# Performance work log

Measured on AMD Instinct MI355X. Metric: run time of the kernel, lower is better.

Reference implementation:

```python
import jax, jax.numpy as jnp
import numpy as np

N_NODES = 50000
N_EDGES = 800000
N_GRAPHS = 512
F_IN = 64
HID = 64
OUT = 1
NUM_LAYERS = 3


def setup_inputs() -> dict:
    key = jax.random.key(0)
    ks = jax.random.split(key, 10)
    x = jax.random.normal(ks[0], (N_NODES, F_IN), dtype=jnp.float32)
    edge_index = jax.random.randint(ks[1], (2, N_EDGES), 0, N_NODES, dtype=jnp.int64)
    batch = jnp.sort(jax.random.randint(ks[2], (N_NODES,), 0, N_GRAPHS, dtype=jnp.int64))
    def glorot(k, shape):
        lim = np.sqrt(6.0 / (shape[0] + shape[1]))
        return jax.random.uniform(k, shape, jnp.float32, -lim, lim)
    W1 = glorot(ks[3], (F_IN, HID))
    b1 = jnp.zeros((HID,), jnp.float32)
    W2 = glorot(ks[4], (HID, HID))
    b2 = jnp.zeros((HID,), jnp.float32)
    Wmem = glorot(ks[5], (HID, OUT))
    bmem = jnp.zeros((OUT,), jnp.float32)
    Wtime = glorot(ks[6], (HID, OUT))
    btime = jnp.zeros((OUT,), jnp.float32)
    return {"x": x, "edge_index": edge_index, "batch": batch,
            "W1": W1, "b1": b1, "W2": W2, "b2": b2,
            "Wmem": Wmem, "bmem": bmem, "Wtime": Wtime, "btime": btime}


def _gcn_forward(x, edge_index, batch, W1, b1, W2, b2, Wmem, bmem, Wtime, btime):
    N = x.shape[0]
    # add self-loops (PyG GCNConv default)
    loop = jnp.arange(N, dtype=edge_index.dtype)
    src = jnp.concatenate([edge_index[0], loop])  # [E+N]
    dst = jnp.concatenate([edge_index[1], loop])
    # symmetric normalization: deg over destination nodes (incl. self-loops)
    deg = jax.ops.segment_sum(jnp.ones_like(dst, dtype=x.dtype), dst, num_segments=N)
    dinv = jnp.where(deg > 0, jax.lax.rsqrt(deg), 0.0)
    norm = (dinv[src] * dinv[dst])[:, None]  # [E+N, 1]

    def conv(h, W, b):
        h = h @ W                                   # transform first (PyG order)
        msg = h[src] * norm                         # gather + normalize
        agg = jax.ops.segment_sum(msg, dst, num_segments=N)  # scatter-add
        return agg + b

    h = jax.nn.relu(conv(x, W1, b1))
    for _ in range(NUM_LAYERS - 1):
        h = jax.nn.relu(conv(h, W2, b2))

    # global_mean_pool over batch index
    sums = jax.ops.segment_sum(h, batch, num_segments=N_GRAPHS)
    cnts = jax.ops.segment_sum(jnp.ones((N,), h.dtype), batch, num_segments=N_GRAPHS)
    pooled = sums / jnp.maximum(cnts, 1.0)[:, None]  # [G, HID]

    mem_pred = (pooled @ Wmem + bmem).squeeze()
    time_pred = (pooled @ Wtime + btime).squeeze()
    return mem_pred, time_pred


def reference(x, edge_index, batch, W1, b1, W2, b2, Wmem, bmem, Wtime, btime):
    return _gcn_forward(x, edge_index, batch, W1, b1, W2, b2, Wmem, bmem, Wtime, btime)
```

## Files before the change

kernel.cpp:

```cpp
#include <hip/hip_runtime.h>
#include <hip/hip_bf16.h>
#include <hip/hip_fp16.h>

#define F 64
#define BSH 7
#define MAXB 512
#define CAPB 4096

typedef short short8 __attribute__((ext_vector_type(8)));
typedef float f32x4  __attribute__((ext_vector_type(4)));

__device__ __forceinline__ unsigned short f2bf(float x) {
    unsigned u = __float_as_uint(x);
    unsigned r = (u + 0x7fff + ((u >> 16) & 1)) >> 16;
    return (unsigned short)r;
}
__device__ __forceinline__ float bf2f(unsigned short h) {
    return __uint_as_float(((unsigned)h) << 16);
}

__global__ void k_prep(const float* __restrict__ W1, const float* __restrict__ W2,
                       short* __restrict__ Wh1, short* __restrict__ Wl1,
                       short* __restrict__ Wh2, short* __restrict__ Wl2,
                       int* __restrict__ bfill,
                       __half* __restrict__ xn, __half* __restrict__ hA,
                       __half* __restrict__ hB, int n,
                       float* __restrict__ pooled, int* __restrict__ cnt, int ng) {
    int b = blockIdx.x, t = threadIdx.x;
    if (b < 4) {
        const float* W = (b < 2) ? W1 : W2;
        short* WhF = (b < 2) ? Wh1 : Wh2;
        short* WlF = (b < 2) ? Wl1 : Wl2;
        int i = (b & 1) * 256 + t;
        int lane = i & 63;
        int ct = i >> 6;
        int tt = ct & 1, c = ct >> 1;
        int j  = c * 16 + (lane & 15);
        int k0 = tt * 32 + (lane >> 4) * 8;
        #pragma unroll
        for (int e = 0; e < 8; ++e) {
            float xv = W[(k0 + e) * F + j];
            unsigned short hi = f2bf(xv);
            WhF[i * 8 + e] = (short)hi;
            WlF[i * 8 + e] = (short)f2bf(xv - bf2f(hi));
        }
    } else if (b == 4) {
        bfill[t]       = t * CAPB;
        bfill[t + 256] = (t + 256) * CAPB;
    } else if (b == 5) {
        if (t < 32)      ((unsigned*)(xn + (size_t)n * F))[t]      = 0u;
        else if (t < 64) ((unsigned*)(hA + (size_t)n * F))[t - 32] = 0u;
        else if (t < 96) ((unsigned*)(hB + (size_t)n * F))[t - 64] = 0u;
    } else {
        int idx = (b - 6) * 256 + t;
        if (idx < ng * F) pooled[idx] = 0.f;
        else if (idx < ng * F + ng) cnt[idx - ng * F] = 0;
    }
}

__global__ void k_binscatter(const int* __restrict__ src, const int* __restrict__ dst,
                             int e, int nbkt, int* __restrict__ bucket_fill,
                             int* __restrict__ binned) {
    __shared__ int h[MAXB], base[MAXB];
    int t = threadIdx.x;
    int perblk = (e + gridDim.x - 1) / gridDim.x;
    int e0 = blockIdx.x * perblk;
    int e1 = min(e0 + perblk, e);
    for (int i = t; i < nbkt; i += 256) h[i] = 0;
    __syncthreads();
    for (int i = e0 + t; i < e1; i += 256) atomicAdd(&h[dst[i] >> BSH], 1);
    __syncthreads();
    for (int i = t; i < nbkt; i += 256) {
        int c = h[i];
        base[i] = c ? atomicAdd(&bucket_fill[i], c) : 0;
        h[i] = 0;
    }
    __syncthreads();
    for (int i = e0 + t; i < e1; i += 256) {
        int d = dst[i];
        int b = d >> BSH;
        int r = atomicAdd(&h[b], 1);
        binned[base[b] + r] = (src[i] << BSH) | (d & ((1 << BSH) - 1));
    }
}

__global__ void k_bincsr(const int* __restrict__ binned, const int* __restrict__ bfill,
                         const float* __restrict__ x, int n,
                         int* __restrict__ csr, int2* __restrict__ rowse,
                         float* __restrict__ dinv, __half* __restrict__ xn) {
    __shared__ int deg[1 << BSH], dp[1 << BSH], rp[1 << BSH], fill[1 << BSH];
    __shared__ int csr_l[CAPB];
    __shared__ int ovf;
    int b = blockIdx.x;
    int t = threadIdx.x;
    int n0 = b << BSH;
    int nn = min(n - n0, 1 << BSH);
    if (nn <= 0) return;
    int base = b * CAPB;
    int cnt = bfill[b] - base;
    if (t < (1 << BSH)) { deg[t] = 0; fill[t] = 0; }
    for (int i = t; i < CAPB; i += 256) csr_l[i] = n;
    __syncthreads();
    for (int i = t; i < cnt; i += 256) atomicAdd(&deg[binned[base + i] & ((1 << BSH) - 1)], 1);
    __syncthreads();
    if (t < 128) { dp[t] = (deg[t] + 15) & ~15; rp[t] = dp[t]; }
    __syncthreads();
    for (int off = 1; off < 128; off <<= 1) {
        int u = 0;
        if (t < 128 && t >= off) u = rp[t - off];
        __syncthreads();
        if (t < 128) rp[t] += u;
        __syncthreads();
    }
    if (t == 0) ovf = (rp[127] > CAPB);
    __syncthreads();
    if (ovf) {
        if (t < 128) { dp[t] = deg[t]; rp[t] = deg[t]; }
        __syncthreads();
        for (int off = 1; off < 128; off <<= 1) {
            int u = 0;
            if (t < 128 && t >= off) u = rp[t - off];
            __syncthreads();
            if (t < 128) rp[t] += u;
            __syncthreads();
        }
    }
    int total = rp[127];
    for (int i = t; i < cnt; i += 256) {
        int pr = binned[base + i];
        int d = pr & ((1 << BSH) - 1);
        int pos = rp[d] - dp[d] + atomicAdd(&fill[d], 1);
        csr_l[pos] = pr >> BSH;
    }
    __syncthreads();
    for (int i = t; i < total; i += 256) csr[base + i] = csr_l[i];
    if (t < nn) {
        int start = base + rp[t] - dp[t];
        rowse[n0 + t] = make_int2(start, start + dp[t]);
        dinv[n0 + t]  = rsqrtf((float)(deg[t] + 1));
    }
    for (int i = t; i < nn * 32; i += 256) {
        int r = i >> 5, l = i & 31;
        float dv = rsqrtf((float)(deg[r] + 1));
        float2 v = ((const float2*)(x + (size_t)(n0 + r) * F))[l];
        ((__half2*)(xn + (size_t)(n0 + r) * F))[l] = __floats2half2_rn(v.x * dv, v.y * dv);
    }
}

template<int SCALE_OUT>
__global__ __launch_bounds__(256, 8)
void k_layer(const __half* __restrict__ Hn, const int2* __restrict__ rowse,
             const int* __restrict__ csr, const float* __restrict__ dinv,
             const short* __restrict__ WhF, const short* __restrict__ WlF,
             const float* __restrict__ bias, __half* __restrict__ out, int n) {
    __shared__ short Ah[16][72];
    __shared__ short Al[16][72];
    __shared__ float sdinv[16];
    int t  = threadIdx.x;
    int w  = t >> 6, t6 = t & 63;
    int g  = t6 >> 5, l = t6 & 31;
    int nb0 = blockIdx.x * 16;
    const __half2* rows = (const __half2*)Hn;

    for (int q = 0; q < 4; ++q) {
        int ndl = w * 4 + q;
        int nd  = nb0 + ndl;
        float ax[8], ay[8];
        #pragma unroll
        for (int i = 0; i < 8; ++i) { ax[i] = 0.f; ay[i] = 0.f; }
        float dn = 0.f;
        if (nd < n) {
            dn = dinv[nd];
            if (g == 0) {
                float2 f = __half22float2(rows[((size_t)nd << 5) + l]);
                ax[0] = f.x; ay[0] = f.y;
            }
            int2 se = rowse[nd];
            int e = se.x, e1 = se.y;
            if ((e & 15) == 0) {
                for (; e + 16 <= e1; e += 16) {
                    const int4* cp = (const int4*)(csr + e + 8 * g);
                    int4 c0 = cp[0], c1 = cp[1];
                    int s[8] = {c0.x, c0.y, c0.z, c0.w, c1.x, c1.y, c1.z, c1.w};
                    #pragma unroll
                    for (int i = 0; i < 8; ++i) {
                        float2 f = __half22float2(rows[((size_t)s[i] << 5) + l]);
                        ax[i] += f.x; ay[i] += f.y;
                    }
                }
            }
            if (g == 0) {
                for (; e < e1; ++e) {
                    int s = csr[e];
                    float2 f = __half22float2(rows[((size_t)s << 5) + l]);
                    ax[7] += f.x; ay[7] += f.y;
                }
            }
        }
        float sx = ((ax[0] + ax[1]) + (ax[2] + ax[3])) + ((ax[4] + ax[5]) + (ax[6] + ax[7]));
        float sy = ((ay[0] + ay[1]) + (ay[2] + ay[3])) + ((ay[4] + ay[5]) + (ay[6] + ay[7]));
        sx += __shfl_xor(sx, 32);
        sy += __shfl_xor(sy, 32);
        sx *= dn; sy *= dn;
        if (g == 0) {
            unsigned short hx = f2bf(sx), hy = f2bf(sy);
            *(unsigned*)&Ah[ndl][2 * l] = (unsigned)hx | ((unsigned)hy << 16);
            unsigned short lx = f2bf(sx - bf2f(hx)), ly = f2bf(sy - bf2f(hy));
            *(unsigned*)&Al[ndl][2 * l] = (unsigned)lx | ((unsigned)ly << 16);
            if (l == 0) sdinv[ndl] = dn;
        }
    }
    __syncthreads();

    int c  = w;
    int jj = t6 & 15;
    int kg = t6 >> 4;
    const short8* WhP = (const short8*)WhF;
    const short8* WlP = (const short8*)WlF;
    short8 bh0 = WhP[(c * 2 + 0) * 64 + t6];
    short8 bh1 = WhP[(c * 2 + 1) * 64 + t6];
    short8 bl0 = WlP[(c * 2 + 0) * 64 + t6];
    short8 bl1 = WlP[(c * 2 + 1) * 64 + t6];
    short8 ah0 = *(const short8*)&Ah[jj][kg * 8];
    short8 ah1 = *(const short8*)&Ah[jj][32 + kg * 8];
    short8 al0 = *(const short8*)&Al[jj][kg * 8];
    short8 al1 = *(const short8*)&Al[jj][32 + kg * 8];

    float bv = bias[c * 16 + jj];
    f32x4 acc = {bv, bv, bv, bv};
    acc = __builtin_amdgcn_mfma_f32_16x16x32_bf16(ah0, bh0, acc, 0, 0, 0);
    acc = __builtin_amdgcn_mfma_f32_16x16x32_bf16(ah1, bh1, acc, 0, 0, 0);
    acc = __builtin_amdgcn_mfma_f32_16x16x32_bf16(al0, bh0, acc, 0, 0, 0);
    acc = __builtin_amdgcn_mfma_f32_16x16x32_bf16(al1, bh1, acc, 0, 0, 0);
    acc = __builtin_amdgcn_mfma_f32_16x16x32_bf16(ah0, bl0, acc, 0, 0, 0);
    acc = __builtin_amdgcn_mfma_f32_16x16x32_bf16(ah1, bl1, acc, 0, 0, 0);

    #pragma unroll
    for (int v = 0; v < 4; ++v) {
        int rr = kg * 4 + v;
        int nd = nb0 + rr;
        if (nd < n) {
            float val = fmaxf(acc[v], 0.f);
            if (SCALE_OUT) val *= sdinv[rr];
            out[(size_t)nd * F + c * 16 + jj] = __float2half(val);
        }
    }
}


#define POOL_C 32
__global__ void k_pool(const __half* __restrict__ h, const int* __restrict__ batch,
                       float* __restrict__ pooled, int* __restrict__ cnt, int n) {
    int wave = (blockIdx.x * blockDim.x + threadIdx.x) >> 6;
    int j = threadIdx.x & 63;
    int n0 = wave * POOL_C;
    if (n0 >= n) return;
    int n1 = min(n0 + POOL_C, n);
    int curg = batch[n0];
    float acc = 0.f; int c = 0;
    for (int i = n0; i < n1; ++i) {
        int g = batch[i];
        if (g != curg) {
            atomicAdd(&pooled[curg * F + j], acc);
            if (j == 0) atomicAdd(&cnt[curg], c);
            curg = g; acc = 0.f; c = 0;
        }
        acc += __half2float(h[(size_t)i * F + j]);
        ++c;
    }
    atomicAdd(&pooled[curg * F + j], acc);
    if (j == 0) atomicAdd(&cnt[curg], c);
}

__global__ void k_head(const float* __restrict__ pooled, const int* __restrict__ cnt,
                       const float* __restrict__ Wm, const float* __restrict__ bm,
                       const float* __restrict__ Wt, const float* __restrict__ bt,
                       float* __restrict__ out, int g) {
    int gid = (blockIdx.x * blockDim.x + threadIdx.x) >> 6;
    int j = threadIdx.x & 63;
    if (gid >= g) return;
    float c = fmaxf((float)cnt[gid], 1.f);
    float p = pooled[gid * F + j] / c;
    float m = p * Wm[j];
    float t = p * Wt[j];
    #pragma unroll
    for (int off = 32; off > 0; off >>= 1) {
        m += __shfl_down(m, off);
        t += __shfl_down(t, off);
    }
    if (j == 0) {
        out[gid]     = m + bm[0];
        out[g + gid] = t + bt[0];
    }
}


static inline size_t alignup(size_t x) { return (x + 255) & ~(size_t)255; }

extern "C" void kernel_launch(void* const* d_in, const int* in_sizes, int n_in,
                              void* d_out, int out_size, void* d_ws, size_t ws_size,
                              hipStream_t stream) {
    const float* x     = (const float*)d_in[0];
    const int*   eidx  = (const int*)d_in[1];
    const int*   batch = (const int*)d_in[2];
    const float* W1    = (const float*)d_in[3];
    const float* b1    = (const float*)d_in[4];
    const float* W2    = (const float*)d_in[5];
    const float* b2    = (const float*)d_in[6];
    const float* Wm    = (const float*)d_in[7];
    const float* bm    = (const float*)d_in[8];
    const float* Wt    = (const float*)d_in[9];
    const float* bt    = (const float*)d_in[10];
    float* out = (float*)d_out;

    const int N = in_sizes[0] / F;
    const int E = in_sizes[1] / 2;
    const int G = out_size / 2;
    const int* src = eidx;
    const int* dst = eidx + E;
    const int nbkt = (N + (1 << BSH) - 1) >> BSH;

    char* p = (char*)d_ws;
    float*  dinv   = (float*)p;  p += alignup(sizeof(float) * N);
    int2*   rowse  = (int2*)p;   p += alignup(sizeof(int2) * N);
    int*    bfill  = (int*)p;    p += alignup(sizeof(int) * MAXB);
    short*  Wh1    = (short*)p;  p += alignup(sizeof(short) * 4096);
    short*  Wl1    = (short*)p;  p += alignup(sizeof(short) * 4096);
    short*  Wh2    = (short*)p;  p += alignup(sizeof(short) * 4096);
    short*  Wl2    = (short*)p;  p += alignup(sizeof(short) * 4096);
    int*    csr    = (int*)p;    p += alignup(sizeof(int) * (size_t)nbkt * CAPB);
    int*    binned = (int*)p;    p += alignup(sizeof(int) * (size_t)nbkt * CAPB);
    __half* xn     = (__half*)p; p += alignup(sizeof(__half) * (size_t)(N + 1) * F);
    __half* hA     = (__half*)p; p += alignup(sizeof(__half) * (size_t)(N + 1) * F);
    __half* hB     = (__half*)p; p += alignup(sizeof(__half) * (size_t)(N + 1) * F);
    float*  pooled = (float*)p;  p += alignup(sizeof(float) * G * F);
    int*    cnt    = (int*)p;    p += alignup(sizeof(int) * G);

    const int TB = 256;

    int gPrep = 6 + (G * F + G + TB - 1) / TB;
    k_prep<<<gPrep, TB, 0, stream>>>(W1, W2, Wh1, Wl1, Wh2, Wl2, bfill,
                                     xn, hA, hB, N, pooled, cnt, G);

    k_binscatter<<<128, TB, 0, stream>>>(src, dst, E, nbkt, bfill, binned);
    k_bincsr    <<<nbkt, TB, 0, stream>>>(binned, bfill, x, N, csr, rowse, dinv, xn);

    int gT = (N + 15) / 16;
    k_layer<1><<<gT, TB, 0, stream>>>(xn, rowse, csr, dinv, Wh1, Wl1, b1, hA, N);
    k_layer<1><<<gT, TB, 0, stream>>>(hA, rowse, csr, dinv, Wh2, Wl2, b2, hB, N);
    k_layer<0><<<gT, TB, 0, stream>>>(hB, rowse, csr, dinv, Wh2, Wl2, b2, hA, N);

    int pw = (N + POOL_C - 1) / POOL_C;
    k_pool<<<(pw * 64 + TB - 1) / TB, TB, 0, stream>>>(hA, batch, pooled, cnt, N);
    int gH = (G * F + TB - 1) / TB;
    k_head<<<gH, TB, 0, stream>>>(pooled, cnt, Wm, bm, Wt, bt, out, G);
}
```

Baseline: 136.7 us.

## Fuse mean pooling into last GCN layer and store CSR indices as uint16

The final layer kernel now applies ReLU, stages its 16 output rows in shared memory and atomically adds per-graph sums and counts. This removes the separate pooling kernel and the write and re-read of the last hidden state. The CSR neighbor indices are also narrowed from 32-bit to 16-bit, halving index traffic in the gather loops. The narrowing only holds while the node count stays below 65536, and the fused pooling issues more atomics per graph than the old pooling kernel did.

```diff
diff --git a/kernel.cpp b/kernel.cpp
--- a/kernel.cpp
+++ b/kernel.cpp
@@ -9,6 +9,7 @@
 
 typedef short short8 __attribute__((ext_vector_type(8)));
 typedef float f32x4  __attribute__((ext_vector_type(4)));
+typedef unsigned short ushort_t;
 
 __device__ __forceinline__ unsigned short f2bf(float x) {
     unsigned u = __float_as_uint(x);
@@ -86,7 +87,7 @@
 
 __global__ void k_bincsr(const int* __restrict__ binned, const int* __restrict__ bfill,
                          const float* __restrict__ x, int n,
-                         int* __restrict__ csr, int2* __restrict__ rowse,
+                         ushort_t* __restrict__ csr, int2* __restrict__ rowse,
                          float* __restrict__ dinv, __half* __restrict__ xn) {
     __shared__ int deg[1 << BSH], dp[1 << BSH], rp[1 << BSH], fill[1 << BSH];
     __shared__ int csr_l[CAPB];
@@ -133,7 +134,7 @@
         csr_l[pos] = pr >> BSH;
     }
     __syncthreads();
-    for (int i = t; i < total; i += 256) csr[base + i] = csr_l[i];
+    for (int i = t; i < total; i += 256) csr[base + i] = (ushort_t)csr_l[i];
     if (t < nn) {
         int start = base + rp[t] - dp[t];
         rowse[n0 + t] = make_int2(start, start + dp[t]);
@@ -147,14 +148,20 @@
     }
 }
 
-template<int SCALE_OUT>
+union SMem {
+    struct { short Ah[16][72]; short Al[16][72]; };
+    struct { float vals[16][68]; int bids[16]; };
+};
+
+template<int MODE>
 __global__ __launch_bounds__(256, 8)
 void k_layer(const __half* __restrict__ Hn, const int2* __restrict__ rowse,
-             const int* __restrict__ csr, const float* __restrict__ dinv,
+             const ushort_t* __restrict__ csr, const float* __restrict__ dinv,
              const short* __restrict__ WhF, const short* __restrict__ WlF,
-             const float* __restrict__ bias, __half* __restrict__ out, int n) {
-    __shared__ short Ah[16][72];
-    __shared__ short Al[16][72];
+             const float* __restrict__ bias, __half* __restrict__ out,
+             const int* __restrict__ batch, float* __restrict__ pooled,
+             int* __restrict__ cnt, int n) {
+    __shared__ SMem sm;
     __shared__ float sdinv[16];
     int t  = threadIdx.x;
     int w  = t >> 6, t6 = t & 63;
@@ -179,9 +186,11 @@
             int e = se.x, e1 = se.y;
             if ((e & 15) == 0) {
                 for (; e + 16 <= e1; e += 16) {
-                    const int4* cp = (const int4*)(csr + e + 8 * g);
-                    int4 c0 = cp[0], c1 = cp[1];
-                    int s[8] = {c0.x, c0.y, c0.z, c0.w, c1.x, c1.y, c1.z, c1.w};
+                    int4 cw = *(const int4*)(csr + e + 8 * g);
+                    int s[8] = { cw.x & 0xffff, (int)((unsigned)cw.x >> 16),
+                                 cw.y & 0xffff, (int)((unsigned)cw.y >> 16),
+                                 cw.z & 0xffff, (int)((unsigned)cw.z >> 16),
+                                 cw.w & 0xffff, (int)((unsigned)cw.w >> 16) };
                     #pragma unroll
                     for (int i = 0; i < 8; ++i) {
                         float2 f = __half22float2(rows[((size_t)s[i] << 5) + l]);
@@ -204,9 +213,9 @@
         sx *= dn; sy *= dn;
         if (g == 0) {
             unsigned short hx = f2bf(sx), hy = f2bf(sy);
-            *(unsigned*)&Ah[ndl][2 * l] = (unsigned)hx | ((unsigned)hy << 16);
+            *(unsigned*)&sm.Ah[ndl][2 * l] = (unsigned)hx | ((unsigned)hy << 16);
             unsigned short lx = f2bf(sx - bf2f(hx)), ly = f2bf(sy - bf2f(hy));
-            *(unsigned*)&Al[ndl][2 * l] = (unsigned)lx | ((unsigned)ly << 16);
+            *(unsigned*)&sm.Al[ndl][2 * l] = (unsigned)lx | ((unsigned)ly << 16);
             if (l == 0) sdinv[ndl] = dn;
         }
     }
@@ -221,10 +230,10 @@
     short8 bh1 = WhP[(c * 2 + 1) * 64 + t6];
     short8 bl0 = WlP[(c * 2 + 0) * 64 + t6];
     short8 bl1 = WlP[(c * 2 + 1) * 64 + t6];
-    short8 ah0 = *(const short8*)&Ah[jj][kg * 8];
-    short8 ah1 = *(const short8*)&Ah[jj][32 + kg * 8];
-    short8 al0 = *(const short8*)&Al[jj][kg * 8];
-    short8 al1 = *(const short8*)&Al[jj][32 + kg * 8];
+    short8 ah0 = *(const short8*)&sm.Ah[jj][kg * 8];
+    short8 ah1 = *(const short8*)&sm.Ah[jj][32 + kg * 8];
+    short8 al0 = *(const short8*)&sm.Al[jj][kg * 8];
+    short8 al1 = *(const short8*)&sm.Al[jj][32 + kg * 8];
 
     float bv = bias[c * 16 + jj];
     f32x4 acc = {bv, bv, bv, bv};
@@ -235,42 +244,51 @@
     acc = __builtin_amdgcn_mfma_f32_16x16x32_bf16(ah0, bl0, acc, 0, 0, 0);
     acc = __builtin_amdgcn_mfma_f32_16x16x32_bf16(ah1, bl1, acc, 0, 0, 0);
 
-    #pragma unroll
-    for (int v = 0; v < 4; ++v) {
-        int rr = kg * 4 + v;
-        int nd = nb0 + rr;
-        if (nd < n) {
-            float val = fmaxf(acc[v], 0.f);
-            if (SCALE_OUT) val *= sdinv[rr];
-            out[(size_t)nd * F + c * 16 + jj] = __float2half(val);
-        }
-    }
-}
-
-
-#define POOL_C 32
-__global__ void k_pool(const __half* __restrict__ h, const int* __restrict__ batch,
-                       float* __restrict__ pooled, int* __restrict__ cnt, int n) {
-    int wave = (blockIdx.x * blockDim.x + threadIdx.x) >> 6;
-    int j = threadIdx.x & 63;
-    int n0 = wave * POOL_C;
-    if (n0 >= n) return;
-    int n1 = min(n0 + POOL_C, n);
-    int curg = batch[n0];
-    float acc = 0.f; int c = 0;
-    for (int i = n0; i < n1; ++i) {
-        int g = batch[i];
-        if (g != curg) {
-            atomicAdd(&pooled[curg * F + j], acc);
-            if (j == 0) atomicAdd(&cnt[curg], c);
-            curg = g; acc = 0.f; c = 0;
-        }
-        acc += __half2float(h[(size_t)i * F + j]);
-        ++c;
-    }
-    atomicAdd(&pooled[curg * F + j], acc);
-    if (j == 0) atomicAdd(&cnt[curg], c);
-}
+    if (MODE == 1) {
+        #pragma unroll
+        for (int v = 0; v < 4; ++v) {
+            int rr = kg * 4 + v;
+            int nd = nb0 + rr;
+            if (nd < n) {
+                float val = fmaxf(acc[v], 0.f) * sdinv[rr];
+                out[(size_t)nd * F + c * 16 + jj] = __float2half(val);
+            }
+        }
+    } else {
+        __syncthreads();
+        #pragma unroll
+        for (int v = 0; v < 4; ++v) {
+            int rr = kg * 4 + v;
+            sm.vals[rr][c * 16 + jj] = fmaxf(acc[v], 0.f);
+        }
+        if (t < 16) sm.bids[t] = (nb0 + t < n) ? batch[nb0 + t] : -1;
+        __syncthreads();
+        if (t < 64) {
+            float accp = 0.f;
+            int curg = sm.bids[0];
+            for (int r = 0; r < 16; ++r) {
+                int g2 = sm.bids[r];
+                if (g2 < 0) break;
+                if (g2 != curg) {
+                    atomicAdd(&pooled[curg * F + t], accp);
+                    curg = g2; accp = 0.f;
+                }
+                accp += sm.vals[r][t];
+            }
+            if (curg >= 0) atomicAdd(&pooled[curg * F + t], accp);
+        } else if (t == 64) {
+            int curg = sm.bids[0], cl = 0;
+            for (int r = 0; r < 16; ++r) {
+                int g2 = sm.bids[r];
+                if (g2 < 0) break;
+                if (g2 != curg) { atomicAdd(&cnt[curg], cl); curg = g2; cl = 0; }
+                ++cl;
+            }
+            if (curg >= 0 && cl) atomicAdd(&cnt[curg], cl);
+        }
+    }
+}
+
 
 __global__ void k_head(const float* __restrict__ pooled, const int* __restrict__ cnt,
                        const float* __restrict__ Wm, const float* __restrict__ bm,
@@ -321,20 +339,20 @@
     const int nbkt = (N + (1 << BSH) - 1) >> BSH;
 
     char* p = (char*)d_ws;
-    float*  dinv   = (float*)p;  p += alignup(sizeof(float) * N);
-    int2*   rowse  = (int2*)p;   p += alignup(sizeof(int2) * N);
-    int*    bfill  = (int*)p;    p += alignup(sizeof(int) * MAXB);
-    short*  Wh1    = (short*)p;  p += alignup(sizeof(short) * 4096);
-    short*  Wl1    = (short*)p;  p += alignup(sizeof(short) * 4096);
-    short*  Wh2    = (short*)p;  p += alignup(sizeof(short) * 4096);
-    short*  Wl2    = (short*)p;  p += alignup(sizeof(short) * 4096);
-    int*    csr    = (int*)p;    p += alignup(sizeof(int) * (size_t)nbkt * CAPB);
-    int*    binned = (int*)p;    p += alignup(sizeof(int) * (size_t)nbkt * CAPB);
-    __half* xn     = (__half*)p; p += alignup(sizeof(__half) * (size_t)(N + 1) * F);
-    __half* hA     = (__half*)p; p += alignup(sizeof(__half) * (size_t)(N + 1) * F);
-    __half* hB     = (__half*)p; p += alignup(sizeof(__half) * (size_t)(N + 1) * F);
-    float*  pooled = (float*)p;  p += alignup(sizeof(float) * G * F);
-    int*    cnt    = (int*)p;    p += alignup(sizeof(int) * G);
+    float*    dinv   = (float*)p;    p += alignup(sizeof(float) * N);
+    int2*     rowse  = (int2*)p;     p += alignup(sizeof(int2) * N);
+    int*      bfill  = (int*)p;      p += alignup(sizeof(int) * MAXB);
+    short*    Wh1    = (short*)p;    p += alignup(sizeof(short) * 4096);
+    short*    Wl1    = (short*)p;    p += alignup(sizeof(short) * 4096);
+    short*    Wh2    = (short*)p;    p += alignup(sizeof(short) * 4096);
+    short*    Wl2    = (short*)p;    p += alignup(sizeof(short) * 4096);
+    ushort_t* csr    = (ushort_t*)p; p += alignup(sizeof(ushort_t) * (size_t)nbkt * CAPB);
+    int*      binned = (int*)p;      p += alignup(sizeof(int) * (size_t)nbkt * CAPB);
+    __half*   xn     = (__half*)p;   p += alignup(sizeof(__half) * (size_t)(N + 1) * F);
+    __half*   hA     = (__half*)p;   p += alignup(sizeof(__half) * (size_t)(N + 1) * F);
+    __half*   hB     = (__half*)p;   p += alignup(sizeof(__half) * (size_t)(N + 1) * F);
+    float*    pooled = (float*)p;    p += alignup(sizeof(float) * G * F);
+    int*      cnt    = (int*)p;      p += alignup(sizeof(int) * G);
 
     const int TB = 256;
 
@@ -346,12 +364,13 @@
     k_bincsr    <<<nbkt, TB, 0, stream>>>(binned, bfill, x, N, csr, rowse, dinv, xn);
 
     int gT = (N + 15) / 16;
-    k_layer<1><<<gT, TB, 0, stream>>>(xn, rowse, csr, dinv, Wh1, Wl1, b1, hA, N);
-    k_layer<1><<<gT, TB, 0, stream>>>(hA, rowse, csr, dinv, Wh2, Wl2, b2, hB, N);
-    k_layer<0><<<gT, TB, 0, stream>>>(hB, rowse, csr, dinv, Wh2, Wl2, b2, hA, N);
-
-    int pw = (N + POOL_C - 1) / POOL_C;
-    k_pool<<<(pw * 64 + TB - 1) / TB, TB, 0, stream>>>(hA, batch, pooled, cnt, N);
+    k_layer<1><<<gT, TB, 0, stream>>>(xn, rowse, csr, dinv, Wh1, Wl1, b1, hA,
+                                      batch, pooled, cnt, N);
+    k_layer<1><<<gT, TB, 0, stream>>>(hA, rowse, csr, dinv, Wh2, Wl2, b2, hB,
+                                      batch, pooled, cnt, N);
+    k_layer<0><<<gT, TB, 0, stream>>>(hB, rowse, csr, dinv, Wh2, Wl2, b2, hA,
+                                      batch, pooled, cnt, N);
+
     int gH = (G * F + TB - 1) / TB;
     k_head<<<gH, TB, 0, stream>>>(pooled, cnt, Wm, bm, Wt, bt, out, G);
 }
```

Measured after the change: 123.1 us. -10.0%, faster.
